# Kernel optimization log

Hardware: AMD Instinct MI355X
Metric: run time of the kernel (lower is better)

Reference implementation:

```python
import jax, jax.numpy as jnp
import numpy as np

TOP_K = 2


def setup_inputs() -> dict:
    key = jax.random.key(0)
    ks = jax.random.split(key, 10)
    B, S, H, E = 4, 2048, 1024, 8
    s = 1.0 / np.sqrt(H)
    x = jax.random.normal(ks[0], (B, S, H), dtype=jnp.float32)
    gate_w = jax.random.normal(ks[1], (H, E), dtype=jnp.float32) * s
    gate_b = jnp.zeros((E,), dtype=jnp.float32)
    w1 = jax.random.normal(ks[2], (E, H, H), dtype=jnp.float32) * s
    b1 = jnp.zeros((E, H), dtype=jnp.float32)
    w2 = jax.random.normal(ks[3], (E, H, H), dtype=jnp.float32) * s
    b2 = jnp.zeros((E, H), dtype=jnp.float32)
    w3 = jax.random.normal(ks[4], (E, H, H), dtype=jnp.float32) * s
    b3 = jnp.zeros((E, H), dtype=jnp.float32)
    return {"x": x, "gate_w": gate_w, "gate_b": gate_b,
            "w1": w1, "b1": b1, "w2": w2, "b2": b2, "w3": w3, "b3": b3}


def reference(x, gate_w, gate_b, w1, b1, w2, b2, w3, b3):
    B, S, H = x.shape
    t = x.reshape(-1, H)                                  # [T, H]
    T = t.shape[0]
    # Router: logits -> fp32 softmax -> top-k -> renormalize
    router_logits = t @ gate_w + gate_b                   # [T, E]
    probs = jax.nn.softmax(router_logits.astype(jnp.float32), axis=-1)
    w, idx = jax.lax.top_k(probs, TOP_K)                  # [T, K]
    w = w / jnp.sum(w, axis=-1, keepdims=True)
    w = w.astype(x.dtype)
    # Dense combine weights: cw[t, e] = router weight if expert e selected for token t, else 0
    rows = jnp.arange(T)[:, None]
    cw = jnp.zeros(router_logits.shape, dtype=x.dtype).at[rows, idx].add(w)  # [T, E]
    # Expert MLPs (relu(fc1) -> relu(fc2) -> fc3), batched over experts
    h1 = jax.nn.relu(jnp.einsum('th,ehf->etf', t, w1) + b1[:, None, :])
    h2 = jax.nn.relu(jnp.einsum('etf,efg->etg', h1, w2) + b2[:, None, :])
    y = jnp.einsum('etg,egh->eth', h2, w3) + b3[:, None, :]                 # [E, T, H]
    # Weighted combine (equivalent to per-expert gather + weighted index_add)
    out = jnp.einsum('te,eth->th', cw, y)                 # [T, H]
    return out.reshape(B, S, H), router_logits
```

## Files before the change

kernel.cpp:

```cpp
#include <hip/hip_runtime.h>
#include <hip/hip_bf16.h>


#define HDIM 1024
#define NEXP 8
#define BM 128
#define BN 128
#define BK 32
#define HH ((size_t)HDIM * HDIM)

typedef __hip_bfloat16 bf16;
typedef unsigned short ushort_t;
typedef __attribute__((ext_vector_type(8))) short bf16x8;
typedef __attribute__((ext_vector_type(4))) float f32x4;

__device__ __forceinline__ float bflo(unsigned u) { return __uint_as_float(u << 16); }
__device__ __forceinline__ float bfhi(unsigned u) { return __uint_as_float(u & 0xffff0000u); }
__device__ __forceinline__ unsigned short f2bfu(float f) {
  bf16 h = __float2bfloat16(f);
  return *reinterpret_cast<unsigned short*>(&h);
}
__device__ __forceinline__ int iclamp(int v, int lo, int hi) {
  return v < lo ? lo : (v > hi ? hi : v);
}

__device__ __forceinline__ void async_cp16(const void* g, void* l) {
  __builtin_amdgcn_global_load_lds((const __attribute__((address_space(1))) void*)g,
                                   (__attribute__((address_space(3))) void*)l,
                                   16, 0, 0);
}

__device__ __forceinline__ void ld4f(const void* base, size_t idx, bool f32, float o[4]) {
  if (f32) {
    float4 v = *(const float4*)((const float*)base + idx);
    o[0] = v.x; o[1] = v.y; o[2] = v.z; o[3] = v.w;
  } else {
    uint2 v = *(const uint2*)((const unsigned short*)base + idx);
    o[0] = bflo(v.x); o[1] = bfhi(v.x); o[2] = bflo(v.y); o[3] = bfhi(v.y);
  }
}

__global__ void k_init(int* __restrict__ meta) {
  int i = blockIdx.x * blockDim.x + threadIdx.x;
  if (i < 3072) meta[i] = 0;
}

__global__ void k_sniff(const ushort_t* a0, int n0, const ushort_t* a1, int n1,
                        const ushort_t* a2, int n2, const ushort_t* a3, int n3,
                        const ushort_t* a4, int n4, int* __restrict__ flags) {
  int b = blockIdx.x;
  const ushort_t* a = b == 0 ? a0 : b == 1 ? a1 : b == 2 ? a2 : b == 3 ? a3 : a4;
  int n = b == 0 ? n0 : b == 1 ? n1 : b == 2 ? n2 : b == 3 ? n3 : n4;
  int hits = 0;
  for (int i = threadIdx.x; i < n; i += 256) {
    ushort_t v = a[i];
    if ((v & 0x7F80) == 0x7F80) hits++;
  }
  if (hits) atomicAdd(&flags[b], hits);
}

__global__ __launch_bounds__(512) void k_router(
    const void* __restrict__ x, const void* __restrict__ gw,
    const bf16* __restrict__ gb, void* __restrict__ dout, bf16* __restrict__ xb,
    int* __restrict__ sel_e, float* __restrict__ sel_w,
    int* __restrict__ meta, int TS, int T) {
  __shared__ float sgT[NEXP][HDIM];
  const int* flags = meta + 2048;
  bool fx = flags[0] != 0, fgw = flags[1] != 0;
  int tid = threadIdx.x;

#pragma unroll
  for (int r = 0; r < 2; r++) {
    int h = r * 512 + tid;
    float g[8];
    ld4f(gw, (size_t)h * NEXP, fgw, g);
    ld4f(gw, (size_t)h * NEXP + 4, fgw, g + 4);
#pragma unroll
    for (int e = 0; e < NEXP; e++) sgT[e][h] = g[e];
  }
  __syncthreads();

  int wave = tid >> 6, lane = tid & 63;
  int t = blockIdx.x * 8 + wave;

  double acc[NEXP];
#pragma unroll
  for (int e = 0; e < NEXP; e++) acc[e] = 0.0;

  if (t < T) {
#pragma unroll
    for (int j = 0; j < 4; j++) {
      int h = j * 256 + lane * 4;
      float xf[4];
      ld4f(x, (size_t)t * HDIM + h, fx, xf);
      if (fx) {
        uint2 ov;
        ov.x = (unsigned)f2bfu(xf[0]) | ((unsigned)f2bfu(xf[1]) << 16);
        ov.y = (unsigned)f2bfu(xf[2]) | ((unsigned)f2bfu(xf[3]) << 16);
        *(uint2*)((unsigned short*)xb + (size_t)t * HDIM + h) = ov;
      }
#pragma unroll
      for (int e = 0; e < NEXP; e++) {
        float4 g = *(const float4*)&sgT[e][h];
        acc[e] += (double)xf[0] * (double)g.x + (double)xf[1] * (double)g.y
                + (double)xf[2] * (double)g.z + (double)xf[3] * (double)g.w;
      }
    }
  }

#pragma unroll
  for (int off = 32; off >= 1; off >>= 1) {
#pragma unroll
    for (int e = 0; e < NEXP; e++) acc[e] += __shfl_down(acc[e], off);
  }

  if (lane == 0 && t < T) {
    double l[NEXP];
#pragma unroll
    for (int e = 0; e < NEXP; e++) l[e] = acc[e] + (double)__bfloat162float(gb[e]);
    size_t lo = (size_t)T * HDIM + (size_t)t * NEXP;
    if (fx) {
      float* lp = (float*)dout + lo;
#pragma unroll
      for (int e = 0; e < NEXP; e++) lp[e] = (float)l[e];
    } else {
      unsigned short* lp = (unsigned short*)dout + lo;
#pragma unroll
      for (int e = 0; e < NEXP; e++) lp[e] = f2bfu((float)l[e]);
    }
    int i1 = 0; double v1 = l[0];
#pragma unroll
    for (int e = 1; e < NEXP; e++) if (l[e] > v1) { v1 = l[e]; i1 = e; }
    int i2 = -1; double v2 = -1e300;
#pragma unroll
    for (int e = 0; e < NEXP; e++) if (e != i1 && l[e] > v2) { v2 = l[e]; i2 = e; }
    if (i2 < 0) i2 = (i1 + 1) & 7;
    float w1 = 1.0f / (1.0f + __expf((float)(v2 - v1)));
    sel_e[2 * t] = i1; sel_e[2 * t + 1] = i2;
    sel_w[2 * t] = w1; sel_w[2 * t + 1] = 1.0f - w1;
  }
}

__global__ void k_offsets(const int* __restrict__ sel_e, int* __restrict__ meta,
                          int* __restrict__ list, int* __restrict__ row_e,
                          int RCAP, int NTMAX, int TS) {
  int s = blockIdx.x;
  __shared__ int base[NEXP + 1];
  __shared__ int wsum[4][NEXP];
  int tid = threadIdx.x;

  int cnt[NEXP];
#pragma unroll
  for (int e = 0; e < NEXP; e++) cnt[e] = 0;
  const int* se = sel_e + (size_t)2 * s * TS;
  for (int i = tid; i < 2 * TS; i += 256) {
    int v = se[i];
#pragma unroll
    for (int e = 0; e < NEXP; e++) cnt[e] += (v == e) ? 1 : 0;
  }
#pragma unroll
  for (int off = 32; off >= 1; off >>= 1)
#pragma unroll
    for (int e = 0; e < NEXP; e++) cnt[e] += __shfl_down(cnt[e], off);
  int lane = tid & 63, wave = tid >> 6;
  if (lane == 0) {
#pragma unroll
    for (int e = 0; e < NEXP; e++) wsum[wave][e] = cnt[e];
  }
  __syncthreads();

  if (tid == 0) {
    int b = 0;
    for (int e = 0; e < NEXP; e++) {
      int ce = wsum[0][e] + wsum[1][e] + wsum[2][e] + wsum[3][e];
      base[e] = b;
      meta[s * 8 + e] = ce;
      meta[512 + s * 8 + e] = b;
      meta[1024 + s * 8 + e] = b;
      b = (b + ce + BM - 1) & ~(BM - 1);
    }
    base[NEXP] = b;
    meta[2560 + s] = b / BM;
  }
  __syncthreads();

  for (int r = tid; r < NTMAX; r += blockDim.x) {
    int rs = r * BM;
    int e = 0;
    for (int q = 1; q < NEXP; q++) if (rs >= base[q]) e = q;
    row_e[s * NTMAX + r] = e;
  }
  int* ls = list + (size_t)s * RCAP;
  for (int e = 0; e < NEXP; e++) {
    int ce = wsum[0][e] + wsum[1][e] + wsum[2][e] + wsum[3][e];
    for (int p = base[e] + ce + tid; p < base[e + 1]; p += blockDim.x)
      ls[p] = s * TS;
  }
}

__global__ void k_scatter(const int* __restrict__ sel_e, int* __restrict__ meta,
                          int* __restrict__ list, int* __restrict__ pos_of,
                          int T, int TS, int RCAP) {
  __shared__ int lcnt[NEXP];
  __shared__ int lbase[NEXP];
  int tid = threadIdx.x;
  if (tid < NEXP) lcnt[tid] = 0;
  __syncthreads();
  int t = blockIdx.x * blockDim.x + tid;
  int s = (int)(((long long)blockIdx.x * blockDim.x) / TS);
  int e0 = sel_e[2 * t], e1 = sel_e[2 * t + 1];
  int r0 = atomicAdd(&lcnt[e0], 1);
  int r1 = atomicAdd(&lcnt[e1], 1);
  __syncthreads();
  if (tid < NEXP) lbase[tid] = atomicAdd(&meta[512 + s * 8 + tid], lcnt[tid]);
  __syncthreads();
  int p0 = lbase[e0] + r0;
  int p1 = lbase[e1] + r1;
  if (p0 >= 0 && p0 < RCAP) list[(size_t)s * RCAP + p0] = t;
  if (p1 >= 0 && p1 < RCAP) list[(size_t)s * RCAP + p1] = t;
  pos_of[2 * t] = p0;
  pos_of[2 * t + 1] = p1;
}

__global__ void k_trans(const void* __restrict__ w, const int* __restrict__ flags,
                        int fidx, bf16* __restrict__ wt) {
  int e = blockIdx.z;
  bool fW = flags[fidx] != 0;
  __shared__ unsigned short tile[32][33];
  int tid = threadIdx.x;
  int r = tid >> 3, c4 = (tid & 7) * 4;
  int R0 = blockIdx.y * 32, C0 = blockIdx.x * 32;
  float v[4];
  ld4f(w, (size_t)e * HH + (size_t)(R0 + r) * HDIM + C0 + c4, fW, v);
  tile[c4 + 0][r] = f2bfu(v[0]);
  tile[c4 + 1][r] = f2bfu(v[1]);
  tile[c4 + 2][r] = f2bfu(v[2]);
  tile[c4 + 3][r] = f2bfu(v[3]);
  __syncthreads();
  uint2 ov;
  ov.x = (unsigned)tile[r][c4 + 0] | ((unsigned)tile[r][c4 + 1] << 16);
  ov.y = (unsigned)tile[r][c4 + 2] | ((unsigned)tile[r][c4 + 3] << 16);
  *(uint2*)((unsigned short*)wt + (size_t)e * HH + (size_t)(C0 + r) * HDIM + R0 + c4) = ov;
}

template <bool GATHER, bool RELU>
__global__ __launch_bounds__(256) void k_gemm(
    const bf16* __restrict__ A, const bf16* __restrict__ Axb,
    const int* __restrict__ list,
    const int* __restrict__ row_e, const int* __restrict__ ntiles,
    const bf16* __restrict__ wt, const bf16* __restrict__ bias,
    bf16* __restrict__ C, const int* __restrict__ flags, int Tm1) {
  int id = blockIdx.y * gridDim.x + blockIdx.x;
  int tm = id % gridDim.y;
  int tn = id / gridDim.y;
  if (tm >= *ntiles) return;
  int e = row_e[tm];
  int row0 = tm * BM;
  const bf16* Ause = (GATHER && flags[0] != 0) ? Axb : A;

  __shared__ __align__(16) unsigned short lA[2 * BM * BK];
  __shared__ __align__(16) unsigned short lB[2 * BN * BK];

  int tid = threadIdx.x;
  int lane = tid & 63, wave = tid >> 6;
  int ksw = ((lane & 3) ^ ((lane >> 3) & 3)) * 8;
  int r0 = wave * 32 + (lane >> 2);

  const unsigned short* pb0 = (const unsigned short*)wt + (size_t)e * HH
                            + (size_t)(tn * BN + r0) * HDIM + ksw;
  const unsigned short* pb1 = pb0 + (size_t)16 * HDIM;
  const unsigned short* pa0;
  const unsigned short* pa1;
  if (GATHER) {
    int t0 = iclamp(list[row0 + r0], 0, Tm1);
    int t1 = iclamp(list[row0 + r0 + 16], 0, Tm1);
    pa0 = (const unsigned short*)Ause + (size_t)t0 * HDIM + ksw;
    pa1 = (const unsigned short*)Ause + (size_t)t1 * HDIM + ksw;
  } else {
    pa0 = (const unsigned short*)Ause + (size_t)(row0 + r0) * HDIM + ksw;
    pa1 = pa0 + (size_t)16 * HDIM;
  }
  unsigned short* laD0 = lA + (wave * 32) * BK;
  unsigned short* laD1 = laD0 + 16 * BK;
  unsigned short* lbD0 = lB + (wave * 32) * BK;
  unsigned short* lbD1 = lbD0 + 16 * BK;

#define STAGE(pb, ktt)                                         \
  do {                                                         \
    int _o = (pb) * (BM * BK);                                 \
    async_cp16(pa0 + (size_t)(ktt) * BK, laD0 + _o);           \
    async_cp16(pa1 + (size_t)(ktt) * BK, laD1 + _o);           \
    async_cp16(pb0 + (size_t)(ktt) * BK, lbD0 + _o);           \
    async_cp16(pb1 + (size_t)(ktt) * BK, lbD1 + _o);           \
  } while (0)

  f32x4 acc[4][4];
#pragma unroll
  for (int i = 0; i < 4; i++)
#pragma unroll
    for (int j = 0; j < 4; j++) acc[i][j] = (f32x4){0.f, 0.f, 0.f, 0.f};

  int lm = lane & 15, quad = lane >> 4;
  int am = (wave & 1) * 64, bn = (wave >> 1) * 64;
  int rdc = (quad ^ ((lm >> 1) & 3)) * 8;

  STAGE(0, 0);
  STAGE(1, 1);

  const int NK = HDIM / BK;
  for (int kt = 0; kt < NK; ++kt) {
    int p = kt & 1;
    if (kt < NK - 1) asm volatile("s_waitcnt vmcnt(4)" ::: "memory");
    else             asm volatile("s_waitcnt vmcnt(0)" ::: "memory");
    __builtin_amdgcn_sched_barrier(0);
    __builtin_amdgcn_s_barrier();
    __builtin_amdgcn_sched_barrier(0);

    int o = p * (BM * BK);
    bf16x8 af[4], bfr[4];
#pragma unroll
    for (int i = 0; i < 4; i++)
      af[i] = *(const bf16x8*)&lA[o + (am + i * 16 + lm) * BK + rdc];
#pragma unroll
    for (int j = 0; j < 4; j++)
      bfr[j] = *(const bf16x8*)&lB[o + (bn + j * 16 + lm) * BK + rdc];
    __builtin_amdgcn_s_setprio(1);
#pragma unroll
    for (int i = 0; i < 4; i++)
#pragma unroll
      for (int j = 0; j < 4; j++)
        acc[i][j] = __builtin_amdgcn_mfma_f32_16x16x32_bf16(af[i], bfr[j], acc[i][j], 0, 0, 0);
    __builtin_amdgcn_s_setprio(0);

    __builtin_amdgcn_sched_barrier(0);
    __builtin_amdgcn_s_barrier();
    __builtin_amdgcn_sched_barrier(0);
    if (kt + 2 < NK) STAGE(p, kt + 2);
  }
#undef STAGE

#pragma unroll
  for (int j = 0; j < 4; j++) {
    int col = tn * BN + bn + j * 16 + lm;
    float bv = __bfloat162float(bias[e * HDIM + col]);
#pragma unroll
    for (int i = 0; i < 4; i++) {
      int rowb = row0 + am + i * 16 + quad * 4;
#pragma unroll
      for (int rr = 0; rr < 4; rr++) {
        float v = acc[i][j][rr] + bv;
        if (RELU) v = fmaxf(v, 0.f);
        ((unsigned short*)C)[(size_t)(rowb + rr) * HDIM + col] = f2bfu(v);
      }
    }
  }
}

__global__ void k_combine(const bf16* __restrict__ y, const int* __restrict__ pos_of,
                          const float* __restrict__ sel_w, void* __restrict__ dout,
                          size_t out_elem_off, const int* __restrict__ meta, int Pm1) {
  bool fx = meta[2048] != 0;
  int t = blockIdx.x;
  int tid = threadIdx.x;
  int p0 = iclamp(pos_of[2 * t], 0, Pm1);
  int p1 = iclamp(pos_of[2 * t + 1], 0, Pm1);
  float w0 = sel_w[2 * t], w1 = sel_w[2 * t + 1];
  int h = tid * 4;
  uint2 a = *(const uint2*)((const unsigned short*)y + (size_t)p0 * HDIM + h);
  uint2 b = *(const uint2*)((const unsigned short*)y + (size_t)p1 * HDIM + h);
  float o0 = w0 * bflo(a.x) + w1 * bflo(b.x);
  float o1 = w0 * bfhi(a.x) + w1 * bfhi(b.x);
  float o2 = w0 * bflo(a.y) + w1 * bflo(b.y);
  float o3 = w0 * bfhi(a.y) + w1 * bfhi(b.y);
  size_t off = out_elem_off + (size_t)t * HDIM + h;
  if (fx) {
    float4 ov = { o0, o1, o2, o3 };
    *(float4*)((float*)dout + off) = ov;
  } else {
    uint2 ov;
    ov.x = (unsigned)f2bfu(o0) | ((unsigned)f2bfu(o1) << 16);
    ov.y = (unsigned)f2bfu(o2) | ((unsigned)f2bfu(o3) << 16);
    *(uint2*)((unsigned short*)dout + off) = ov;
  }
}

extern "C" void kernel_launch(void* const* d_in, const int* in_sizes, int n_in,
                              void* d_out, int out_size, void* d_ws, size_t ws_size,
                              hipStream_t stream) {
  const void* x  = d_in[0];
  const void* gw = d_in[1];
  const bf16* gb = (const bf16*)d_in[2];
  const void* w1 = d_in[3];
  const bf16* b1 = (const bf16*)d_in[4];
  const void* w2 = d_in[5];
  const bf16* b2 = (const bf16*)d_in[6];
  const void* w3 = d_in[7];
  const bf16* b3 = (const bf16*)d_in[8];

  const int T = in_sizes[0] / HDIM;
  const size_t wtsz = (size_t)NEXP * HH * 2;
  const size_t xbsz = (size_t)T * HDIM * 2;

  int S = 64;
  size_t base_need = 0;
  for (int cand = 1; cand <= 64; cand *= 2) {
    size_t rcap = (size_t)2 * T / cand + NEXP * BM;
    size_t ntmx = rcap / BM;
    size_t need = 12288 + (size_t)8 * T * 3 + (size_t)4 * cand * rcap
                + (size_t)4 * cand * ntmx + wtsz + 2 * rcap * HDIM * 2
                + xbsz + 1024;
    if (need <= ws_size) { S = cand; base_need = need; break; }
  }
  const int TS = T / S;
  const int RCAP = 2 * TS + NEXP * BM;
  const int NTMAX = RCAP / BM;
  const bool hoist = (S > 1) && (base_need + 2 * wtsz <= ws_size);

  char* ws = (char*)d_ws;
  size_t ofs = 0;
  int*   meta   = (int*)(ws + ofs);   ofs += 12288;
  int*   sel_e  = (int*)(ws + ofs);   ofs += (size_t)8 * T;
  float* sel_w  = (float*)(ws + ofs); ofs += (size_t)8 * T;
  int*   pos_of = (int*)(ws + ofs);   ofs += (size_t)8 * T;
  int*   list   = (int*)(ws + ofs);   ofs += (size_t)4 * S * RCAP;
  int*   row_e  = (int*)(ws + ofs);   ofs += (size_t)4 * S * NTMAX;
  ofs = (ofs + 255) & ~(size_t)255;
  bf16* wt0 = (bf16*)(ws + ofs); ofs += wtsz;
  bf16* h1  = (bf16*)(ws + ofs); ofs += (size_t)RCAP * HDIM * 2;
  bf16* h2  = (bf16*)(ws + ofs); ofs += (size_t)RCAP * HDIM * 2;
  bf16* xb  = (bf16*)(ws + ofs); ofs += xbsz;
  bf16* wt1 = wt0;
  bf16* wt2 = wt0;
  if (hoist) {
    wt1 = (bf16*)(ws + ofs); ofs += wtsz;
    wt2 = (bf16*)(ws + ofs); ofs += wtsz;
  }

  int* flags = meta + 2048;

  k_init<<<12, 256, 0, stream>>>(meta);
  k_sniff<<<5, 256, 0, stream>>>((const ushort_t*)x, 32768,
                                 (const ushort_t*)gw, HDIM * NEXP,
                                 (const ushort_t*)w1, 32768,
                                 (const ushort_t*)w2, 32768,
                                 (const ushort_t*)w3, 32768, flags);
  k_router<<<(T + 7) / 8, 512, 0, stream>>>(x, gw, gb, d_out, xb, sel_e, sel_w,
                                            meta, TS, T);
  k_offsets<<<S, 256, 0, stream>>>(sel_e, meta, list, row_e, RCAP, NTMAX, TS);
  {
    int sbd = TS < 256 ? TS : 256;
    k_scatter<<<T / sbd, sbd, 0, stream>>>(sel_e, meta, list, pos_of, T, TS, RCAP);
  }

  dim3 tg(HDIM / 32, HDIM / 32, NEXP);
  dim3 gg(HDIM / BN, NTMAX);
  const bf16* xbf = (const bf16*)x;

  if (hoist) {
    k_trans<<<tg, 256, 0, stream>>>(w1, flags, 2, wt0);
    k_trans<<<tg, 256, 0, stream>>>(w2, flags, 3, wt1);
    k_trans<<<tg, 256, 0, stream>>>(w3, flags, 4, wt2);
  }
  for (int s = 0; s < S; s++) {
    const int* lst = list + (size_t)s * RCAP;
    const int* re  = row_e + (size_t)s * NTMAX;
    const int* nt  = meta + 2560 + s;
    if (!hoist) k_trans<<<tg, 256, 0, stream>>>(w1, flags, 2, wt0);
    k_gemm<true,  true ><<<gg, 256, 0, stream>>>(xbf, xb, lst, re, nt, wt0, b1, h1, flags, T - 1);
    if (!hoist) k_trans<<<tg, 256, 0, stream>>>(w2, flags, 3, wt1);
    k_gemm<false, true ><<<gg, 256, 0, stream>>>(h1, nullptr, nullptr, re, nt, wt1, b2, h2, flags, T - 1);
    if (!hoist) k_trans<<<tg, 256, 0, stream>>>(w3, flags, 4, wt2);
    k_gemm<false, false><<<gg, 256, 0, stream>>>(h2, nullptr, nullptr, re, nt, wt2, b3, h1, flags, T - 1);
    k_combine<<<TS, 256, 0, stream>>>(h1, pos_of + (size_t)2 * s * TS,
                                      sel_w + (size_t)2 * s * TS,
                                      d_out, (size_t)s * TS * HDIM, meta, RCAP - 1);
  }
}
```

Before: 432.9 us.

## Deepen GEMM LDS pipeline to four stages and stage output through LDS

Changes the expert GEMM's shared-memory ring from two to four buffers, keeping three K-tiles in flight. The next load is issued right after the top barrier, which removes the second barrier in each iteration. The epilogue now writes the bf16 tile into LDS and then stores it to global memory as 16-byte vector stores, replacing scattered 2-byte stores. LDS use doubles to 64KB per block, which may reduce occupancy.

```diff
diff --git a/kernel.cpp b/kernel.cpp
--- a/kernel.cpp
+++ b/kernel.cpp
@@ -258,8 +258,8 @@
   int row0 = tm * BM;
   const bf16* Ause = (GATHER && flags[0] != 0) ? Axb : A;
 
-  __shared__ __align__(16) unsigned short lA[2 * BM * BK];
-  __shared__ __align__(16) unsigned short lB[2 * BN * BK];
+  const int BUF = (BM + BN) * BK;
+  __shared__ __align__(16) unsigned short smem[4 * (BM + BN) * BK];
 
   int tid = threadIdx.x;
   int lane = tid & 63, wave = tid >> 6;
@@ -280,14 +280,14 @@
     pa0 = (const unsigned short*)Ause + (size_t)(row0 + r0) * HDIM + ksw;
     pa1 = pa0 + (size_t)16 * HDIM;
   }
-  unsigned short* laD0 = lA + (wave * 32) * BK;
+  unsigned short* laD0 = smem + (wave * 32) * BK;
   unsigned short* laD1 = laD0 + 16 * BK;
-  unsigned short* lbD0 = lB + (wave * 32) * BK;
+  unsigned short* lbD0 = smem + BM * BK + (wave * 32) * BK;
   unsigned short* lbD1 = lbD0 + 16 * BK;
 
 #define STAGE(pb, ktt)                                         \
   do {                                                         \
-    int _o = (pb) * (BM * BK);                                 \
+    int _o = (pb) * BUF;                                       \
     async_cp16(pa0 + (size_t)(ktt) * BK, laD0 + _o);           \
     async_cp16(pa1 + (size_t)(ktt) * BK, laD1 + _o);           \
     async_cp16(pb0 + (size_t)(ktt) * BK, lbD0 + _o);           \
@@ -306,24 +306,27 @@
 
   STAGE(0, 0);
   STAGE(1, 1);
+  STAGE(2, 2);
 
   const int NK = HDIM / BK;
   for (int kt = 0; kt < NK; ++kt) {
-    int p = kt & 1;
-    if (kt < NK - 1) asm volatile("s_waitcnt vmcnt(4)" ::: "memory");
-    else             asm volatile("s_waitcnt vmcnt(0)" ::: "memory");
+    int p = kt & 3;
+    if (kt < NK - 2)       asm volatile("s_waitcnt vmcnt(8)" ::: "memory");
+    else if (kt == NK - 2) asm volatile("s_waitcnt vmcnt(4)" ::: "memory");
+    else                   asm volatile("s_waitcnt vmcnt(0)" ::: "memory");
     __builtin_amdgcn_sched_barrier(0);
     __builtin_amdgcn_s_barrier();
     __builtin_amdgcn_sched_barrier(0);
-
-    int o = p * (BM * BK);
+    if (kt + 3 < NK) STAGE((kt + 3) & 3, kt + 3);
+
+    int o = p * BUF;
     bf16x8 af[4], bfr[4];
 #pragma unroll
     for (int i = 0; i < 4; i++)
-      af[i] = *(const bf16x8*)&lA[o + (am + i * 16 + lm) * BK + rdc];
+      af[i] = *(const bf16x8*)&smem[o + (am + i * 16 + lm) * BK + rdc];
 #pragma unroll
     for (int j = 0; j < 4; j++)
-      bfr[j] = *(const bf16x8*)&lB[o + (bn + j * 16 + lm) * BK + rdc];
+      bfr[j] = *(const bf16x8*)&smem[o + BM * BK + (bn + j * 16 + lm) * BK + rdc];
     __builtin_amdgcn_s_setprio(1);
 #pragma unroll
     for (int i = 0; i < 4; i++)
@@ -331,27 +334,36 @@
       for (int j = 0; j < 4; j++)
         acc[i][j] = __builtin_amdgcn_mfma_f32_16x16x32_bf16(af[i], bfr[j], acc[i][j], 0, 0, 0);
     __builtin_amdgcn_s_setprio(0);
-
-    __builtin_amdgcn_sched_barrier(0);
-    __builtin_amdgcn_s_barrier();
-    __builtin_amdgcn_sched_barrier(0);
-    if (kt + 2 < NK) STAGE(p, kt + 2);
   }
 #undef STAGE
 
+  __syncthreads();
+  unsigned short* cst = smem;
 #pragma unroll
   for (int j = 0; j < 4; j++) {
-    int col = tn * BN + bn + j * 16 + lm;
-    float bv = __bfloat162float(bias[e * HDIM + col]);
+    int col = bn + j * 16 + lm;
+    float bv = __bfloat162float(bias[e * HDIM + tn * BN + col]);
 #pragma unroll
     for (int i = 0; i < 4; i++) {
-      int rowb = row0 + am + i * 16 + quad * 4;
+      int rowb = am + i * 16 + quad * 4;
 #pragma unroll
       for (int rr = 0; rr < 4; rr++) {
         float v = acc[i][j][rr] + bv;
         if (RELU) v = fmaxf(v, 0.f);
-        ((unsigned short*)C)[(size_t)(rowb + rr) * HDIM + col] = f2bfu(v);
+        cst[(rowb + rr) * BN + col] = f2bfu(v);
       }
+    }
+  }
+  __syncthreads();
+  {
+    unsigned short* Cg = (unsigned short*)C;
+#pragma unroll
+    for (int it = 0; it < 8; it++) {
+      int o = it * 4096 + tid * 16;
+      int row = o >> 8;
+      int cole = (o & 255) >> 1;
+      uint4 v = *(const uint4*)((const char*)cst + o);
+      *(uint4*)&Cg[(size_t)(row0 + row) * HDIM + tn * BN + cole] = v;
     }
   }
 }
```

New measurement: 429.0 us. Within noise of the previous version (-0.9%).
